# Kernel optimization log

Measured on AMD Instinct MI355X. Metric: run time of the kernel, lower is better.

The kernel has to match this reference:

```python
import jax, jax.numpy as jnp
from jax import lax
import numpy as np

B, N, K = 8, 4096, 64          # clouds, points per cloud, max neighbors
N1, N2 = N // 2, N // 8        # fps ratio 0.5, then 0.25
R1, R2 = 0.2, 0.4              # ball-query radii


def setup_inputs() -> dict:
    key = jax.random.key(0)
    ks = jax.random.split(key, 7)
    def w(k, i, o):
        return jax.random.normal(k, (i, o), jnp.float32) / np.sqrt(i).astype(np.float32)
    return {
        "pos": jax.random.uniform(ks[0], (B, N, 3), jnp.float32),
        "w1a": w(ks[1], 3, 64),    "b1a": jnp.zeros(64, jnp.float32),
        "w1b": w(ks[2], 64, 64),   "b1b": jnp.zeros(64, jnp.float32),
        "w2a": w(ks[3], 67, 128),  "b2a": jnp.zeros(128, jnp.float32),
        "w2b": w(ks[4], 128, 128), "b2b": jnp.zeros(128, jnp.float32),
        "w3a": w(ks[5], 131, 256), "b3a": jnp.zeros(256, jnp.float32),
        "w3b": w(ks[6], 256, 1024),"b3b": jnp.zeros(1024, jnp.float32),
    }


def fps(pos, n_samples):
    # farthest point sampling, deterministic start at index 0. pos: [n, 3]
    d0 = jnp.sum((pos - pos[0]) ** 2, axis=-1)
    def step(mind, _):
        nxt = jnp.argmax(mind)
        d = jnp.sum((pos - pos[nxt]) ** 2, axis=-1)
        return jnp.minimum(mind, d), nxt
    _, idxs = lax.scan(step, d0, None, length=n_samples - 1)
    return jnp.concatenate([jnp.zeros((1,), idxs.dtype), idxs])


def ball_query(centers, pts, r):
    # up to K neighbors within radius r (nearest-first); centers are a subset of pts
    d2 = jnp.sum((centers[:, None, :] - pts[None, :, :]) ** 2, axis=-1)  # [M, n]
    neg = jnp.where(d2 <= r * r, -d2, -jnp.inf)
    vals, nbr = lax.top_k(neg, K)
    return nbr, vals > -jnp.inf  # [M, K] indices, validity mask


def mlp(x, w1, b1, w2, b2, relu_last):
    h = jax.nn.relu(x @ w1 + b1) @ w2 + b2
    return jax.nn.relu(h) if relu_last else h


def masked_max(h, mask):
    # max over neighbor axis; every center has itself as a valid neighbor
    return jnp.max(jnp.where(mask[..., None], h, -jnp.inf), axis=1)


def reference(pos, w1a, b1a, w1b, b1b, w2a, b2a, w2b, b2b, w3a, b3a, w3b, b3b):
    def single(p):  # p: [N, 3]
        # SA1: x is None -> per-edge input is relative position only
        idx1 = fps(p, N1)
        c1 = p[idx1]                                   # [N1, 3]
        nbr1, m1 = ball_query(c1, p, R1)               # [N1, K]
        rel1 = p[nbr1] - c1[:, None, :]                # [N1, K, 3]
        x1 = masked_max(mlp(rel1, w1a, b1a, w1b, b1b, True), m1)   # [N1, 64]
        # SA2: per-edge input is [x_j, pos_j - pos_i]
        idx2 = fps(c1, N2)
        c2 = c1[idx2]                                  # [N2, 3]
        nbr2, m2 = ball_query(c2, c1, R2)              # [N2, K]
        feat2 = jnp.concatenate([x1[nbr2], c1[nbr2] - c2[:, None, :]], axis=-1)  # [N2,K,67]
        x2 = masked_max(mlp(feat2, w2a, b2a, w2b, b2b, True), m2)  # [N2, 128]
        # Global SA: MLP on [x, pos] then global max pool
        g = mlp(jnp.concatenate([x2, c2], axis=-1), w3a, b3a, w3b, b3b, False)   # [N2,1024]
        return jnp.max(g, axis=0)                      # [1024]
    return jax.vmap(single)(pos)                       # [B, 1024]
```

## Files before the change

### kernel.cpp

```cpp
#include <hip/hip_runtime.h>
#include <cstdint>
#include <cstddef>


static constexpr int Bc = 8;
static constexpr int Np = 4096;
static constexpr int Kn = 64;
static constexpr int M1 = 2048;
static constexpr int M2 = 512;
static constexpr int LDX = 132;

#define DEVINL __device__ __forceinline__

DEVINL float d2_exact(float ax, float ay, float az, float bx, float by, float bz) {
    float dx = __fsub_rn(ax, bx);
    float dy = __fsub_rn(ay, by);
    float dz = __fsub_rn(az, bz);
    float xx = __fmul_rn(dx, dx);
    float yy = __fmul_rn(dy, dy);
    float zz = __fmul_rn(dz, dz);
    return __fadd_rn(__fadd_rn(xx, yy), zz);
}

DEVINL unsigned long long wave_max_u64(unsigned long long k) {
    #pragma unroll
    for (int o = 32; o > 0; o >>= 1) {
        unsigned long long other = __shfl_xor(k, o, 64);
        if (other > k) k = other;
    }
    return k;
}

template <int N>
__global__ __launch_bounds__(256)
void fps_kernel(const float* __restrict__ pts, int ns,
                int* __restrict__ idx_out, float* __restrict__ cent) {
    constexpr int PT = N / 256;
    __shared__ float sx_[N], sy_[N], sz_[N];
    __shared__ unsigned long long pbuf[2][4];
    const int b = blockIdx.x;
    const int t = threadIdx.x;
    const int wid = t >> 6;
    const int lane = t & 63;
    const float* base = pts + (size_t)b * N * 3;

    float px[PT], py[PT], pz[PT], mind[PT];
    #pragma unroll
    for (int j = 0; j < PT; ++j) {
        int p = j * 256 + t;
        px[j] = base[p * 3 + 0];
        py[j] = base[p * 3 + 1];
        pz[j] = base[p * 3 + 2];
        sx_[p] = px[j]; sy_[p] = py[j]; sz_[p] = pz[j];
    }
    float x0 = base[0], y0 = base[1], z0 = base[2];
    float bv = -1.0f; int bi = 0;
    #pragma unroll
    for (int j = 0; j < PT; ++j) {
        float d = d2_exact(px[j], py[j], pz[j], x0, y0, z0);
        mind[j] = d;
        if (d > bv) { bv = d; bi = j * 256 + t; }
    }
    unsigned long long key = ((unsigned long long)__float_as_uint(bv) << 32)
                           | (unsigned long long)(0xFFFFFFFFu - (unsigned)bi);
    key = wave_max_u64(key);
    if (lane == 0) pbuf[1][wid] = key;
    if (t == 0) {
        idx_out[(size_t)b * ns] = 0;
        cent[((size_t)b * ns) * 3 + 0] = x0;
        cent[((size_t)b * ns) * 3 + 1] = y0;
        cent[((size_t)b * ns) * 3 + 2] = z0;
    }
    for (int s = 1; s < ns; ++s) {
        __syncthreads();
        unsigned long long k0 = pbuf[s & 1][0];
        unsigned long long k1 = pbuf[s & 1][1];
        unsigned long long k2 = pbuf[s & 1][2];
        unsigned long long k3 = pbuf[s & 1][3];
        unsigned long long ka = k0 > k1 ? k0 : k1;
        unsigned long long kb = k2 > k3 ? k2 : k3;
        unsigned long long km = ka > kb ? ka : kb;
        int idx = (int)(0xFFFFFFFFu - (unsigned)(km & 0xFFFFFFFFull));
        float cx = sx_[idx], cy = sy_[idx], cz = sz_[idx];
        if (t == 0) {
            idx_out[(size_t)b * ns + s] = idx;
            cent[((size_t)b * ns + s) * 3 + 0] = cx;
            cent[((size_t)b * ns + s) * 3 + 1] = cy;
            cent[((size_t)b * ns + s) * 3 + 2] = cz;
        }
        bv = -1.0f; bi = 0;
        #pragma unroll
        for (int j = 0; j < PT; ++j) {
            float d = d2_exact(px[j], py[j], pz[j], cx, cy, cz);
            float m = fminf(mind[j], d);
            mind[j] = m;
            if (m > bv) { bv = m; bi = j * 256 + t; }
        }
        key = ((unsigned long long)__float_as_uint(bv) << 32)
            | (unsigned long long)(0xFFFFFFFFu - (unsigned)bi);
        key = wave_max_u64(key);
        if (lane == 0) pbuf[(s + 1) & 1][wid] = key;
    }
}

template <int NPT>
__global__ __launch_bounds__(256)
void bq_kernel(const float* __restrict__ pts, const float* __restrict__ ctr,
               int mshift, float r2, int* __restrict__ nbr) {
    constexpr int CH = NPT / 64;
    const int lane = threadIdx.x & 63;
    int w = __builtin_amdgcn_readfirstlane((int)(blockIdx.x * 4 + (threadIdx.x >> 6)));
    const int b = w >> mshift;
    const float* pb = pts + (size_t)b * NPT * 3;
    const float* cp = ctr + (size_t)w * 3;
    float cx = cp[0], cy = cp[1], cz = cp[2];
    const unsigned r2b = __float_as_uint(r2);

    unsigned ub[CH];
    int cnt = 0;
    #pragma unroll
    for (int j = 0; j < CH; ++j) {
        int p = j * 64 + lane;
        float d = d2_exact(pb[p * 3 + 0], pb[p * 3 + 1], pb[p * 3 + 2], cx, cy, cz);
        ub[j] = __float_as_uint(d);
        cnt += __popcll(__ballot(ub[j] <= r2b));
    }
    int* out = nbr + (size_t)w * Kn;
    const unsigned long long lml = (1ull << lane) - 1ull;

    if (cnt <= Kn) {
        int basep = 0;
        #pragma unroll
        for (int j = 0; j < CH; ++j) {
            bool v = ub[j] <= r2b;
            unsigned long long mk = __ballot(v);
            if (v) out[basep + __popcll(mk & lml)] = j * 64 + lane;
            basep += __popcll(mk);
        }
        if (lane >= cnt) out[lane] = -1;
    } else {
        unsigned lo = 0, hi = r2b;
        while (lo < hi) {
            unsigned mid = lo + ((hi - lo) >> 1);
            int c = 0;
            #pragma unroll
            for (int j = 0; j < CH; ++j) c += __popcll(__ballot(ub[j] <= mid));
            if (c >= Kn) hi = mid; else lo = mid + 1;
        }
        const unsigned tt = lo;
        int cntLess = 0;
        #pragma unroll
        for (int j = 0; j < CH; ++j) cntLess += __popcll(__ballot(ub[j] < tt));
        const int quota = Kn - cntLess;
        int baseLt = 0, eqseen = 0;
        #pragma unroll
        for (int j = 0; j < CH; ++j) {
            bool lt = ub[j] < tt;
            bool eq = ub[j] == tt;
            unsigned long long mlt = __ballot(lt);
            unsigned long long meq = __ballot(eq);
            if (lt) out[baseLt + __popcll(mlt & lml)] = j * 64 + lane;
            if (eq) {
                int rr = eqseen + __popcll(meq & lml);
                if (rr < quota) out[cntLess + rr] = j * 64 + lane;
            }
            baseLt += __popcll(mlt);
            eqseen += __popcll(meq);
        }
    }
}

__global__ __launch_bounds__(256)
void mlp1_kernel(const float* __restrict__ pos, const float* __restrict__ c1,
                 const int* __restrict__ nbr, const float* __restrict__ w1aT,
                 const float* __restrict__ w1bT, const float* __restrict__ b1b,
                 float* __restrict__ x1) {
    const int lane = threadIdx.x & 63;
    int w = __builtin_amdgcn_readfirstlane((int)(blockIdx.x * 4 + (threadIdx.x >> 6)));
    const int b = w >> 11;
    const int ii = nbr[(size_t)w * Kn + lane];
    const bool valid = ii >= 0;
    const int i2 = valid ? ii : 0;
    const float* pp = pos + ((size_t)b * Np + i2) * 3;
    const float* cc = c1 + (size_t)w * 3;
    float rx = pp[0] - cc[0], ry = pp[1] - cc[1], rz = pp[2] - cc[2];
    float h1[64];
    #pragma unroll
    for (int h = 0; h < 64; ++h) {
        float4 wv = ((const float4*)w1aT)[h];
        float a = fmaf(rx, wv.x, fmaf(ry, wv.y, fmaf(rz, wv.z, wv.w)));
        h1[h] = fmaxf(a, 0.0f);
    }
    float* orow = x1 + (size_t)w * 64;
    for (int c4 = 0; c4 < 16; ++c4) {
        float v4[4];
        #pragma unroll
        for (int cq = 0; cq < 4; ++cq) {
            int c = c4 * 4 + cq;
            float acc = b1b[c];
            const float4* wr = (const float4*)(w1bT + (size_t)c * 64);
            #pragma unroll
            for (int q = 0; q < 16; ++q) {
                float4 wv = wr[q];
                acc = fmaf(h1[4 * q + 0], wv.x, acc);
                acc = fmaf(h1[4 * q + 1], wv.y, acc);
                acc = fmaf(h1[4 * q + 2], wv.z, acc);
                acc = fmaf(h1[4 * q + 3], wv.w, acc);
            }
            float v = fmaxf(acc, 0.0f);
            v = valid ? v : -__builtin_inff();
            #pragma unroll
            for (int o = 32; o > 0; o >>= 1) v = fmaxf(v, __shfl_xor(v, o, 64));
            v4[cq] = v;
        }
        if (lane == 0)
            ((float4*)orow)[c4] = make_float4(v4[0], v4[1], v4[2], v4[3]);
    }
}

__global__ __launch_bounds__(256)
void mlp2_kernel(const float* __restrict__ x1, const float* __restrict__ c1,
                 const float* __restrict__ c2, const int* __restrict__ nbr2,
                 const float* __restrict__ w2aT, const float* __restrict__ w2bT,
                 const float* __restrict__ b2b, float* __restrict__ X) {
    const int lane = threadIdx.x & 63;
    int w = __builtin_amdgcn_readfirstlane((int)(blockIdx.x * 4 + (threadIdx.x >> 6)));
    const int b = w >> 9;
    const int ii = nbr2[(size_t)w * Kn + lane];
    const bool valid = ii >= 0;
    const int i2 = valid ? ii : 0;

    float x[68];
    const float4* xr = (const float4*)(x1 + ((size_t)b * M1 + i2) * 64);
    #pragma unroll
    for (int q = 0; q < 16; ++q) {
        float4 v = xr[q];
        x[4 * q + 0] = v.x; x[4 * q + 1] = v.y;
        x[4 * q + 2] = v.z; x[4 * q + 3] = v.w;
    }
    const float* cc = c2 + (size_t)w * 3;
    const float* cp = c1 + ((size_t)b * M1 + i2) * 3;
    x[64] = cp[0] - cc[0];
    x[65] = cp[1] - cc[1];
    x[66] = cp[2] - cc[2];
    x[67] = 0.0f;

    float h1[128];
    #pragma unroll
    for (int h = 0; h < 128; ++h) {
        const float4* r4 = (const float4*)(w2aT + (size_t)h * 80);
        float acc = 0.0f;
        #pragma unroll
        for (int q = 0; q < 16; ++q) {
            float4 wv = r4[q];
            acc = fmaf(x[4 * q + 0], wv.x, acc);
            acc = fmaf(x[4 * q + 1], wv.y, acc);
            acc = fmaf(x[4 * q + 2], wv.z, acc);
            acc = fmaf(x[4 * q + 3], wv.w, acc);
        }
        float4 tl = r4[16];
        acc = fmaf(x[64], tl.x, acc);
        acc = fmaf(x[65], tl.y, acc);
        acc = fmaf(x[66], tl.z, acc);
        acc += tl.w;
        h1[h] = fmaxf(acc, 0.0f);
    }
    float* orow = X + (size_t)w * LDX;
    for (int c4 = 0; c4 < 32; ++c4) {
        float v4[4];
        #pragma unroll
        for (int cq = 0; cq < 4; ++cq) {
            int c = c4 * 4 + cq;
            float acc = b2b[c];
            const float4* wr = (const float4*)(w2bT + (size_t)c * 128);
            #pragma unroll
            for (int q = 0; q < 32; ++q) {
                float4 wv = wr[q];
                acc = fmaf(h1[4 * q + 0], wv.x, acc);
                acc = fmaf(h1[4 * q + 1], wv.y, acc);
                acc = fmaf(h1[4 * q + 2], wv.z, acc);
                acc = fmaf(h1[4 * q + 3], wv.w, acc);
            }
            float v = fmaxf(acc, 0.0f);
            v = valid ? v : -__builtin_inff();
            #pragma unroll
            for (int o = 32; o > 0; o >>= 1) v = fmaxf(v, __shfl_xor(v, o, 64));
            v4[cq] = v;
        }
        if (lane == 0) {
            orow[c4 * 4 + 0] = v4[0]; orow[c4 * 4 + 1] = v4[1];
            orow[c4 * 4 + 2] = v4[2]; orow[c4 * 4 + 3] = v4[3];
        }
    }
}

__global__ __launch_bounds__(256)
void writec2_kernel(const float* __restrict__ c2, float* __restrict__ X) {
    int i = blockIdx.x * 256 + threadIdx.x;
    if (i < Bc * M2 * 3) {
        int w = i / 3, d = i - w * 3;
        X[(size_t)w * LDX + 128 + d] = c2[i];
    }
}

__global__ __launch_bounds__(256)
void gemm1_kernel(const float* __restrict__ X, const float* __restrict__ w3a,
                  const float* __restrict__ b3a, float* __restrict__ H) {
    const int r = blockIdx.x;
    const int c = threadIdx.x;
    const float* xr = X + (size_t)r * LDX;
    float acc = b3a[c];
    for (int i = 0; i < 131; ++i)
        acc = fmaf(xr[i], w3a[(size_t)i * 256 + c], acc);
    H[(size_t)r * 256 + c] = fmaxf(acc, 0.0f);
}

__global__ __launch_bounds__(256)
void gemm2_kernel(const float* __restrict__ H, const float* __restrict__ w3b,
                  float* __restrict__ part) {
    __shared__ float As[32][33];
    __shared__ float Bs[32][64];
    __shared__ float red[8][64];
    const int bidx = blockIdx.x;
    const int nt = bidx & 15;
    const int mt = (bidx >> 4) & 15;
    const int b = bidx >> 8;
    const int row0 = b * M2 + mt * 32;
    const int col0 = nt * 64;
    const int t = threadIdx.x;
    const int rg = t >> 5, cg = t & 31;

    float acc[4][2] = {{0.f, 0.f}, {0.f, 0.f}, {0.f, 0.f}, {0.f, 0.f}};
    for (int k0 = 0; k0 < 256; k0 += 32) {
        #pragma unroll
        for (int q = 0; q < 4; ++q) {
            int id = t + q * 256;
            As[id >> 5][id & 31] = H[(size_t)(row0 + (id >> 5)) * 256 + k0 + (id & 31)];
        }
        #pragma unroll
        for (int q = 0; q < 8; ++q) {
            int id = t + q * 256;
            Bs[id >> 6][id & 63] = w3b[(size_t)(k0 + (id >> 6)) * 1024 + col0 + (id & 63)];
        }
        __syncthreads();
        #pragma unroll
        for (int kk = 0; kk < 32; ++kk) {
            float b0 = Bs[kk][cg * 2 + 0];
            float b1 = Bs[kk][cg * 2 + 1];
            #pragma unroll
            for (int j = 0; j < 4; ++j) {
                float a = As[rg * 4 + j][kk];
                acc[j][0] = fmaf(a, b0, acc[j][0]);
                acc[j][1] = fmaf(a, b1, acc[j][1]);
            }
        }
        __syncthreads();
    }
    float m0 = fmaxf(fmaxf(acc[0][0], acc[1][0]), fmaxf(acc[2][0], acc[3][0]));
    float m1 = fmaxf(fmaxf(acc[0][1], acc[1][1]), fmaxf(acc[2][1], acc[3][1]));
    red[rg][cg * 2 + 0] = m0;
    red[rg][cg * 2 + 1] = m1;
    __syncthreads();
    if (t < 64) {
        float v = red[0][t];
        #pragma unroll
        for (int q = 1; q < 8; ++q) v = fmaxf(v, red[q][t]);
        part[((size_t)b * 16 + mt) * 1024 + col0 + t] = v;
    }
}

__global__ __launch_bounds__(256)
void rmax_kernel(const float* __restrict__ part, const float* __restrict__ b3b,
                 float* __restrict__ out) {
    int i = blockIdx.x * 256 + threadIdx.x;
    int b = i >> 10, c = i & 1023;
    float v = -__builtin_inff();
    #pragma unroll
    for (int tt = 0; tt < 16; ++tt)
        v = fmaxf(v, part[((size_t)b * 16 + tt) * 1024 + c]);
    out[i] = v + b3b[c];
}

__global__ __launch_bounds__(256)
void prep_kernel(const float* __restrict__ w1a, const float* __restrict__ b1a,
                 const float* __restrict__ w1b, const float* __restrict__ w2a,
                 const float* __restrict__ b2a, const float* __restrict__ w2b,
                 float* __restrict__ w1aT, float* __restrict__ w1bT,
                 float* __restrict__ w2aT, float* __restrict__ w2bT) {
    int i = blockIdx.x * 256 + threadIdx.x;
    if (i < 64 * 4) {
        int h = i >> 2, d = i & 3;
        w1aT[i] = (d < 3) ? w1a[d * 64 + h] : b1a[h];
    }
    if (i < 64 * 64) {
        int c = i >> 6, h = i & 63;
        w1bT[i] = w1b[h * 64 + c];
    }
    if (i < 128 * 80) {
        int h = i / 80, d = i - h * 80;
        w2aT[i] = (d < 67) ? w2a[d * 128 + h] : ((d == 67) ? b2a[h] : 0.0f);
    }
    {
        int c = i >> 7, h = i & 127;
        w2bT[i] = w2b[h * 128 + c];
    }
}

extern "C" void kernel_launch(void* const* d_in, const int* in_sizes, int n_in,
                              void* d_out, int out_size, void* d_ws, size_t ws_size,
                              hipStream_t stream) {
    const float* pos = (const float*)d_in[0];
    const float* w1a = (const float*)d_in[1];
    const float* b1a = (const float*)d_in[2];
    const float* w1b = (const float*)d_in[3];
    const float* b1b = (const float*)d_in[4];
    const float* w2a = (const float*)d_in[5];
    const float* b2a = (const float*)d_in[6];
    const float* w2b = (const float*)d_in[7];
    const float* b2b = (const float*)d_in[8];
    const float* w3a = (const float*)d_in[9];
    const float* b3a = (const float*)d_in[10];
    const float* w3b = (const float*)d_in[11];
    const float* b3b = (const float*)d_in[12];
    float* out = (float*)d_out;

    char* ws = (char*)d_ws;
    size_t off = 0;
    auto alloc = [&](size_t bytes) -> char* {
        char* p = ws + off;
        off += (bytes + 255) & ~(size_t)255;
        return p;
    };
    float* c1   = (float*)alloc(sizeof(float) * Bc * M1 * 3);
    float* c2   = (float*)alloc(sizeof(float) * Bc * M2 * 3);
    int*   idx1 = (int*)alloc(sizeof(int) * Bc * M1);
    int*   idx2 = (int*)alloc(sizeof(int) * Bc * M2);
    int*   nbr1 = (int*)alloc(sizeof(int) * Bc * M1 * Kn);
    int*   nbr2 = (int*)alloc(sizeof(int) * Bc * M2 * Kn);
    float* x1   = (float*)alloc(sizeof(float) * Bc * M1 * 64);
    float* X    = (float*)alloc(sizeof(float) * Bc * M2 * LDX);
    float* H    = (float*)alloc(sizeof(float) * Bc * M2 * 256);
    float* part = (float*)alloc(sizeof(float) * Bc * 16 * 1024);
    float* w1aT = (float*)alloc(sizeof(float) * 64 * 4);
    float* w1bT = (float*)alloc(sizeof(float) * 64 * 64);
    float* w2aT = (float*)alloc(sizeof(float) * 128 * 80);
    float* w2bT = (float*)alloc(sizeof(float) * 128 * 128);

    prep_kernel<<<dim3(64), dim3(256), 0, stream>>>(w1a, b1a, w1b, w2a, b2a, w2b,
                                                    w1aT, w1bT, w2aT, w2bT);
    fps_kernel<Np><<<dim3(Bc), dim3(256), 0, stream>>>(pos, M1, idx1, c1);
    bq_kernel<Np><<<dim3(Bc * M1 / 4), dim3(256), 0, stream>>>(
        pos, c1, 11, (float)(0.2 * 0.2), nbr1);
    mlp1_kernel<<<dim3(Bc * M1 / 4), dim3(256), 0, stream>>>(
        pos, c1, nbr1, w1aT, w1bT, b1b, x1);
    fps_kernel<M1><<<dim3(Bc), dim3(256), 0, stream>>>(c1, M2, idx2, c2);
    bq_kernel<M1><<<dim3(Bc * M2 / 4), dim3(256), 0, stream>>>(
        c1, c2, 9, (float)(0.4 * 0.4), nbr2);
    mlp2_kernel<<<dim3(Bc * M2 / 4), dim3(256), 0, stream>>>(
        x1, c1, c2, nbr2, w2aT, w2bT, b2b, X);
    writec2_kernel<<<dim3(48), dim3(256), 0, stream>>>(c2, X);
    gemm1_kernel<<<dim3(Bc * M2), dim3(256), 0, stream>>>(X, w3a, b3a, H);
    gemm2_kernel<<<dim3(Bc * 16 * 16), dim3(256), 0, stream>>>(H, w3b, part);
    rmax_kernel<<<dim3(32), dim3(256), 0, stream>>>(part, b3b, out);
}
```

Baseline: 2.787 ms.

## Fuse both FPS stages into one 512-thread kernel with DPP reductions and compacted ball query

Merges the two farthest-point-sampling passes into one kernel per cloud with 512 threads. The winner's coordinates are carried through a DPP-based wave reduction, so the shared-memory lookup of the chosen point after each barrier goes away, and the second stage reads its points straight from LDS. The fused kernel also writes the c2 coordinates into X, which removes the separate writec2 kernel, and the unused index buffers are dropped. Ball query gains a middle path that compacts in-radius candidates into LDS before the binary-search selection, so the search passes only scan the compacted list. The risks are more registers and LDS per block, and a dependence on DPP row broadcast semantics being correct.

```diff
diff --git a/kernel.cpp b/kernel.cpp
--- a/kernel.cpp
+++ b/kernel.cpp
@@ -22,84 +22,206 @@
     return __fadd_rn(__fadd_rn(xx, yy), zz);
 }
 
-DEVINL unsigned long long wave_max_u64(unsigned long long k) {
-    #pragma unroll
-    for (int o = 32; o > 0; o >>= 1) {
-        unsigned long long other = __shfl_xor(k, o, 64);
-        if (other > k) k = other;
-    }
-    return k;
-}
-
-template <int N>
-__global__ __launch_bounds__(256)
-void fps_kernel(const float* __restrict__ pts, int ns,
-                int* __restrict__ idx_out, float* __restrict__ cent) {
-    constexpr int PT = N / 256;
-    __shared__ float sx_[N], sy_[N], sz_[N];
-    __shared__ unsigned long long pbuf[2][4];
+struct Cand { unsigned long long key; float x, y, z; };
+
+DEVINL Cand cmax(Cand a, Cand b) {
+    bool tk = b.key > a.key;
+    Cand r;
+    r.key = tk ? b.key : a.key;
+    r.x = tk ? b.x : a.x;
+    r.y = tk ? b.y : a.y;
+    r.z = tk ? b.z : a.z;
+    return r;
+}
+
+template <int C, int R, int Bm>
+DEVINL Cand dpp_shift(Cand c) {
+    Cand s;
+    unsigned lo = (unsigned)c.key, hi = (unsigned)(c.key >> 32);
+    unsigned slo = (unsigned)__builtin_amdgcn_update_dpp(0, (int)lo, C, R, Bm, true);
+    unsigned shi = (unsigned)__builtin_amdgcn_update_dpp(0, (int)hi, C, R, Bm, true);
+    s.key = ((unsigned long long)shi << 32) | (unsigned long long)slo;
+    s.x = __int_as_float(__builtin_amdgcn_update_dpp(0, __float_as_int(c.x), C, R, Bm, true));
+    s.y = __int_as_float(__builtin_amdgcn_update_dpp(0, __float_as_int(c.y), C, R, Bm, true));
+    s.z = __int_as_float(__builtin_amdgcn_update_dpp(0, __float_as_int(c.z), C, R, Bm, true));
+    return s;
+}
+
+DEVINL Cand wave_max_cand(Cand c) {
+    c = cmax(c, dpp_shift<0x111, 0xf, 0xf>(c));
+    c = cmax(c, dpp_shift<0x112, 0xf, 0xf>(c));
+    c = cmax(c, dpp_shift<0x114, 0xf, 0xf>(c));
+    c = cmax(c, dpp_shift<0x118, 0xf, 0xf>(c));
+    c = cmax(c, dpp_shift<0x142, 0xa, 0xf>(c));
+    c = cmax(c, dpp_shift<0x143, 0xc, 0xf>(c));
+    return c;
+}
+
+DEVINL void sel2(unsigned long long ka, float4 ca, unsigned long long kb, float4 cb,
+                 unsigned long long& ko, float4& co) {
+    bool tk = kb > ka;
+    ko = tk ? kb : ka;
+    co.x = tk ? cb.x : ca.x;
+    co.y = tk ? cb.y : ca.y;
+    co.z = tk ? cb.z : ca.z;
+}
+
+__global__ __launch_bounds__(512)
+void fps2x_kernel(const float* __restrict__ pos, float* __restrict__ c1,
+                  float* __restrict__ c2, float* __restrict__ X) {
+    constexpr int NT = 512;
+    __shared__ float s2x[M1], s2y[M1], s2z[M1];
+    __shared__ alignas(16) unsigned long long pK[2][8];
+    __shared__ alignas(16) float4 pC[2][8];
     const int b = blockIdx.x;
     const int t = threadIdx.x;
     const int wid = t >> 6;
     const int lane = t & 63;
-    const float* base = pts + (size_t)b * N * 3;
-
-    float px[PT], py[PT], pz[PT], mind[PT];
-    #pragma unroll
-    for (int j = 0; j < PT; ++j) {
-        int p = j * 256 + t;
-        px[j] = base[p * 3 + 0];
-        py[j] = base[p * 3 + 1];
-        pz[j] = base[p * 3 + 2];
-        sx_[p] = px[j]; sy_[p] = py[j]; sz_[p] = pz[j];
-    }
-    float x0 = base[0], y0 = base[1], z0 = base[2];
-    float bv = -1.0f; int bi = 0;
-    #pragma unroll
-    for (int j = 0; j < PT; ++j) {
-        float d = d2_exact(px[j], py[j], pz[j], x0, y0, z0);
-        mind[j] = d;
-        if (d > bv) { bv = d; bi = j * 256 + t; }
-    }
-    unsigned long long key = ((unsigned long long)__float_as_uint(bv) << 32)
-                           | (unsigned long long)(0xFFFFFFFFu - (unsigned)bi);
-    key = wave_max_u64(key);
-    if (lane == 0) pbuf[1][wid] = key;
-    if (t == 0) {
-        idx_out[(size_t)b * ns] = 0;
-        cent[((size_t)b * ns) * 3 + 0] = x0;
-        cent[((size_t)b * ns) * 3 + 1] = y0;
-        cent[((size_t)b * ns) * 3 + 2] = z0;
-    }
-    for (int s = 1; s < ns; ++s) {
-        __syncthreads();
-        unsigned long long k0 = pbuf[s & 1][0];
-        unsigned long long k1 = pbuf[s & 1][1];
-        unsigned long long k2 = pbuf[s & 1][2];
-        unsigned long long k3 = pbuf[s & 1][3];
-        unsigned long long ka = k0 > k1 ? k0 : k1;
-        unsigned long long kb = k2 > k3 ? k2 : k3;
-        unsigned long long km = ka > kb ? ka : kb;
-        int idx = (int)(0xFFFFFFFFu - (unsigned)(km & 0xFFFFFFFFull));
-        float cx = sx_[idx], cy = sy_[idx], cz = sz_[idx];
+
+    {
+        constexpr int PT = Np / NT;
+        const float* base = pos + (size_t)b * Np * 3;
+        float px[PT], py[PT], pz[PT], mind[PT];
+        #pragma unroll
+        for (int j = 0; j < PT; ++j) {
+            int p = j * NT + t;
+            px[j] = base[p * 3 + 0];
+            py[j] = base[p * 3 + 1];
+            pz[j] = base[p * 3 + 2];
+        }
+        float x0 = base[0], y0 = base[1], z0 = base[2];
+        float bv = -1.0f, bx = 0.f, by = 0.f, bz = 0.f; int bi = 0;
+        #pragma unroll
+        for (int j = 0; j < PT; ++j) {
+            float d = d2_exact(px[j], py[j], pz[j], x0, y0, z0);
+            mind[j] = d;
+            if (d > bv) { bv = d; bi = j * NT + t; bx = px[j]; by = py[j]; bz = pz[j]; }
+        }
+        Cand c;
+        c.key = ((unsigned long long)__float_as_uint(bv) << 32)
+              | (unsigned long long)(0xFFFFFFFFu - (unsigned)bi);
+        c.x = bx; c.y = by; c.z = bz;
+        c = wave_max_cand(c);
+        if (lane == 63) { pK[1][wid] = c.key; pC[1][wid] = make_float4(c.x, c.y, c.z, 0.f); }
         if (t == 0) {
-            idx_out[(size_t)b * ns + s] = idx;
-            cent[((size_t)b * ns + s) * 3 + 0] = cx;
-            cent[((size_t)b * ns + s) * 3 + 1] = cy;
-            cent[((size_t)b * ns + s) * 3 + 2] = cz;
-        }
-        bv = -1.0f; bi = 0;
+            c1[((size_t)b * M1) * 3 + 0] = x0;
+            c1[((size_t)b * M1) * 3 + 1] = y0;
+            c1[((size_t)b * M1) * 3 + 2] = z0;
+            s2x[0] = x0; s2y[0] = y0; s2z[0] = z0;
+        }
+        for (int s = 1; s < M1; ++s) {
+            __syncthreads();
+            const int rb = s & 1;
+            const ulonglong2* pk2 = (const ulonglong2*)pK[rb];
+            ulonglong2 k01 = pk2[0], k23 = pk2[1], k45 = pk2[2], k67 = pk2[3];
+            float4 q0 = pC[rb][0], q1 = pC[rb][1], q2 = pC[rb][2], q3 = pC[rb][3];
+            float4 q4 = pC[rb][4], q5 = pC[rb][5], q6 = pC[rb][6], q7 = pC[rb][7];
+            unsigned long long m01, m23, m45, m67, ma, mb, mw;
+            float4 s01, s23, s45, s67, sa, sb, sw;
+            sel2(k01.x, q0, k01.y, q1, m01, s01);
+            sel2(k23.x, q2, k23.y, q3, m23, s23);
+            sel2(k45.x, q4, k45.y, q5, m45, s45);
+            sel2(k67.x, q6, k67.y, q7, m67, s67);
+            sel2(m01, s01, m23, s23, ma, sa);
+            sel2(m45, s45, m67, s67, mb, sb);
+            sel2(ma, sa, mb, sb, mw, sw);
+            float cx = sw.x, cy = sw.y, cz = sw.z;
+            if (t == 0) {
+                c1[((size_t)b * M1 + s) * 3 + 0] = cx;
+                c1[((size_t)b * M1 + s) * 3 + 1] = cy;
+                c1[((size_t)b * M1 + s) * 3 + 2] = cz;
+                s2x[s] = cx; s2y[s] = cy; s2z[s] = cz;
+            }
+            bv = -1.0f; bi = 0; bx = 0.f; by = 0.f; bz = 0.f;
+            #pragma unroll
+            for (int j = 0; j < PT; ++j) {
+                float d = d2_exact(px[j], py[j], pz[j], cx, cy, cz);
+                float m = fminf(mind[j], d);
+                mind[j] = m;
+                if (m > bv) { bv = m; bi = j * NT + t; bx = px[j]; by = py[j]; bz = pz[j]; }
+            }
+            c.key = ((unsigned long long)__float_as_uint(bv) << 32)
+                  | (unsigned long long)(0xFFFFFFFFu - (unsigned)bi);
+            c.x = bx; c.y = by; c.z = bz;
+            c = wave_max_cand(c);
+            if (lane == 63) {
+                pK[(s + 1) & 1][wid] = c.key;
+                pC[(s + 1) & 1][wid] = make_float4(c.x, c.y, c.z, 0.f);
+            }
+        }
+    }
+    __syncthreads();
+
+    {
+        constexpr int PT = M1 / NT;
+        float px[PT], py[PT], pz[PT], mind[PT];
         #pragma unroll
         for (int j = 0; j < PT; ++j) {
-            float d = d2_exact(px[j], py[j], pz[j], cx, cy, cz);
-            float m = fminf(mind[j], d);
-            mind[j] = m;
-            if (m > bv) { bv = m; bi = j * 256 + t; }
-        }
-        key = ((unsigned long long)__float_as_uint(bv) << 32)
-            | (unsigned long long)(0xFFFFFFFFu - (unsigned)bi);
-        key = wave_max_u64(key);
-        if (lane == 0) pbuf[(s + 1) & 1][wid] = key;
+            int p = j * NT + t;
+            px[j] = s2x[p]; py[j] = s2y[p]; pz[j] = s2z[p];
+        }
+        float x0 = s2x[0], y0 = s2y[0], z0 = s2z[0];
+        float bv = -1.0f, bx = 0.f, by = 0.f, bz = 0.f; int bi = 0;
+        #pragma unroll
+        for (int j = 0; j < PT; ++j) {
+            float d = d2_exact(px[j], py[j], pz[j], x0, y0, z0);
+            mind[j] = d;
+            if (d > bv) { bv = d; bi = j * NT + t; bx = px[j]; by = py[j]; bz = pz[j]; }
+        }
+        Cand c;
+        c.key = ((unsigned long long)__float_as_uint(bv) << 32)
+              | (unsigned long long)(0xFFFFFFFFu - (unsigned)bi);
+        c.x = bx; c.y = by; c.z = bz;
+        c = wave_max_cand(c);
+        if (lane == 63) { pK[1][wid] = c.key; pC[1][wid] = make_float4(c.x, c.y, c.z, 0.f); }
+        if (t == 0) {
+            c2[((size_t)b * M2) * 3 + 0] = x0;
+            c2[((size_t)b * M2) * 3 + 1] = y0;
+            c2[((size_t)b * M2) * 3 + 2] = z0;
+            float* xr = X + (size_t)(b * M2) * LDX;
+            xr[128] = x0; xr[129] = y0; xr[130] = z0;
+        }
+        for (int s = 1; s < M2; ++s) {
+            __syncthreads();
+            const int rb = s & 1;
+            const ulonglong2* pk2 = (const ulonglong2*)pK[rb];
+            ulonglong2 k01 = pk2[0], k23 = pk2[1], k45 = pk2[2], k67 = pk2[3];
+            float4 q0 = pC[rb][0], q1 = pC[rb][1], q2 = pC[rb][2], q3 = pC[rb][3];
+            float4 q4 = pC[rb][4], q5 = pC[rb][5], q6 = pC[rb][6], q7 = pC[rb][7];
+            unsigned long long m01, m23, m45, m67, ma, mb, mw;
+            float4 s01, s23, s45, s67, sa, sb, sw;
+            sel2(k01.x, q0, k01.y, q1, m01, s01);
+            sel2(k23.x, q2, k23.y, q3, m23, s23);
+            sel2(k45.x, q4, k45.y, q5, m45, s45);
+            sel2(k67.x, q6, k67.y, q7, m67, s67);
+            sel2(m01, s01, m23, s23, ma, sa);
+            sel2(m45, s45, m67, s67, mb, sb);
+            sel2(ma, sa, mb, sb, mw, sw);
+            float cx = sw.x, cy = sw.y, cz = sw.z;
+            if (t == 0) {
+                c2[((size_t)b * M2 + s) * 3 + 0] = cx;
+                c2[((size_t)b * M2 + s) * 3 + 1] = cy;
+                c2[((size_t)b * M2 + s) * 3 + 2] = cz;
+                float* xr = X + (size_t)(b * M2 + s) * LDX;
+                xr[128] = cx; xr[129] = cy; xr[130] = cz;
+            }
+            bv = -1.0f; bi = 0; bx = 0.f; by = 0.f; bz = 0.f;
+            #pragma unroll
+            for (int j = 0; j < PT; ++j) {
+                float d = d2_exact(px[j], py[j], pz[j], cx, cy, cz);
+                float m = fminf(mind[j], d);
+                mind[j] = m;
+                if (m > bv) { bv = m; bi = j * NT + t; bx = px[j]; by = py[j]; bz = pz[j]; }
+            }
+            c.key = ((unsigned long long)__float_as_uint(bv) << 32)
+                  | (unsigned long long)(0xFFFFFFFFu - (unsigned)bi);
+            c.x = bx; c.y = by; c.z = bz;
+            c = wave_max_cand(c);
+            if (lane == 63) {
+                pK[(s + 1) & 1][wid] = c.key;
+                pC[(s + 1) & 1][wid] = make_float4(c.x, c.y, c.z, 0.f);
+            }
+        }
     }
 }
 
@@ -108,8 +230,11 @@
 void bq_kernel(const float* __restrict__ pts, const float* __restrict__ ctr,
                int mshift, float r2, int* __restrict__ nbr) {
     constexpr int CH = NPT / 64;
+    constexpr int CAP = 1024;
+    __shared__ uint2 cbuf[4][CAP];
     const int lane = threadIdx.x & 63;
-    int w = __builtin_amdgcn_readfirstlane((int)(blockIdx.x * 4 + (threadIdx.x >> 6)));
+    const int wl = threadIdx.x >> 6;
+    int w = __builtin_amdgcn_readfirstlane((int)(blockIdx.x * 4 + wl));
     const int b = w >> mshift;
     const float* pb = pts + (size_t)b * NPT * 3;
     const float* cp = ctr + (size_t)w * 3;
@@ -138,6 +263,62 @@
             basep += __popcll(mk);
         }
         if (lane >= cnt) out[lane] = -1;
+    } else if (cnt <= CAP) {
+        uint2* buf = cbuf[wl];
+        int basep = 0;
+        #pragma unroll
+        for (int j = 0; j < CH; ++j) {
+            bool v = ub[j] <= r2b;
+            unsigned long long mk = __ballot(v);
+            if (v) buf[basep + __popcll(mk & lml)] =
+                       make_uint2(ub[j], (unsigned)(j * 64 + lane));
+            basep += __popcll(mk);
+        }
+        const int C2 = (cnt + 63) >> 6;
+        unsigned cb[CAP / 64], ci[CAP / 64];
+        #pragma unroll
+        for (int e = 0; e < CAP / 64; ++e) {
+            if (e >= C2) break;
+            int p = e * 64 + lane;
+            uint2 v = buf[p];
+            cb[e] = (p < cnt) ? v.x : 0xFFFFFFFFu;
+            ci[e] = v.y;
+        }
+        unsigned lo = 0, hi = r2b;
+        while (lo < hi) {
+            unsigned mid = lo + ((hi - lo) >> 1);
+            int c = 0;
+            #pragma unroll
+            for (int e = 0; e < CAP / 64; ++e) {
+                if (e >= C2) break;
+                c += __popcll(__ballot(cb[e] <= mid));
+            }
+            if (c >= Kn) hi = mid; else lo = mid + 1;
+        }
+        const unsigned tt = lo;
+        int cntLess = 0;
+        #pragma unroll
+        for (int e = 0; e < CAP / 64; ++e) {
+            if (e >= C2) break;
+            cntLess += __popcll(__ballot(cb[e] < tt));
+        }
+        const int quota = Kn - cntLess;
+        int baseLt = 0, eqseen = 0;
+        #pragma unroll
+        for (int e = 0; e < CAP / 64; ++e) {
+            if (e >= C2) break;
+            bool lt = cb[e] < tt;
+            bool eq = cb[e] == tt;
+            unsigned long long mlt = __ballot(lt);
+            unsigned long long meq = __ballot(eq);
+            if (lt) out[baseLt + __popcll(mlt & lml)] = (int)ci[e];
+            if (eq) {
+                int rr = eqseen + __popcll(meq & lml);
+                if (rr < quota) out[cntLess + rr] = (int)ci[e];
+            }
+            baseLt += __popcll(mlt);
+            eqseen += __popcll(meq);
+        }
     } else {
         unsigned lo = 0, hi = r2b;
         while (lo < hi) {
@@ -295,15 +476,6 @@
 }
 
 __global__ __launch_bounds__(256)
-void writec2_kernel(const float* __restrict__ c2, float* __restrict__ X) {
-    int i = blockIdx.x * 256 + threadIdx.x;
-    if (i < Bc * M2 * 3) {
-        int w = i / 3, d = i - w * 3;
-        X[(size_t)w * LDX + 128 + d] = c2[i];
-    }
-}
-
-__global__ __launch_bounds__(256)
 void gemm1_kernel(const float* __restrict__ X, const float* __restrict__ w3a,
                   const float* __restrict__ b3a, float* __restrict__ H) {
     const int r = blockIdx.x;
@@ -433,8 +605,6 @@
     };
     float* c1   = (float*)alloc(sizeof(float) * Bc * M1 * 3);
     float* c2   = (float*)alloc(sizeof(float) * Bc * M2 * 3);
-    int*   idx1 = (int*)alloc(sizeof(int) * Bc * M1);
-    int*   idx2 = (int*)alloc(sizeof(int) * Bc * M2);
     int*   nbr1 = (int*)alloc(sizeof(int) * Bc * M1 * Kn);
     int*   nbr2 = (int*)alloc(sizeof(int) * Bc * M2 * Kn);
     float* x1   = (float*)alloc(sizeof(float) * Bc * M1 * 64);
@@ -448,17 +618,15 @@
 
     prep_kernel<<<dim3(64), dim3(256), 0, stream>>>(w1a, b1a, w1b, w2a, b2a, w2b,
                                                     w1aT, w1bT, w2aT, w2bT);
-    fps_kernel<Np><<<dim3(Bc), dim3(256), 0, stream>>>(pos, M1, idx1, c1);
+    fps2x_kernel<<<dim3(Bc), dim3(512), 0, stream>>>(pos, c1, c2, X);
     bq_kernel<Np><<<dim3(Bc * M1 / 4), dim3(256), 0, stream>>>(
         pos, c1, 11, (float)(0.2 * 0.2), nbr1);
     mlp1_kernel<<<dim3(Bc * M1 / 4), dim3(256), 0, stream>>>(
         pos, c1, nbr1, w1aT, w1bT, b1b, x1);
-    fps_kernel<M1><<<dim3(Bc), dim3(256), 0, stream>>>(c1, M2, idx2, c2);
     bq_kernel<M1><<<dim3(Bc * M2 / 4), dim3(256), 0, stream>>>(
         c1, c2, 9, (float)(0.4 * 0.4), nbr2);
     mlp2_kernel<<<dim3(Bc * M2 / 4), dim3(256), 0, stream>>>(
         x1, c1, c2, nbr2, w2aT, w2bT, b2b, X);
-    writec2_kernel<<<dim3(48), dim3(256), 0, stream>>>(c2, X);
     gemm1_kernel<<<dim3(Bc * M2), dim3(256), 0, stream>>>(X, w3a, b3a, H);
     gemm2_kernel<<<dim3(Bc * 16 * 16), dim3(256), 0, stream>>>(H, w3b, part);
     rmax_kernel<<<dim3(32), dim3(256), 0, stream>>>(part, b3b, out);
```

Result: slower. 3.239 ms (+16.2%).
